# Optimization experiments

Measured on AMD Instinct MI355X. Metric: run time of the kernel, lower is better.

The kernel has to match this reference:

```python
import jax, jax.numpy as jnp
import numpy as np

BN_EPS = 1e-5

def conv1x1(x, w, b):
    # x: [B,C,H,W], w: [O,C], b: [O] -> [B,O,H,W]
    return jnp.einsum('bchw,oc->bohw', x, w) + b[None, :, None, None]

def maxpool2x2(x):
    B, C, H, W = x.shape
    return x.reshape(B, C, H // 2, 2, W // 2, 2).max(axis=(3, 5))

def setup_inputs() -> dict:
    key = jax.random.key(0)
    ks = jax.random.split(key, 12)
    B, C, Ci, H, W = 8, 256, 128, 64, 64
    s_in = 1.0 / np.sqrt(C)
    s_mid = 1.0 / np.sqrt(Ci)
    return {
        'x': jax.random.normal(ks[0], (B, C, H, W), jnp.float32),
        'y': jax.random.normal(ks[1], (B, C, H, W), jnp.float32),
        'theta_w': jax.random.normal(ks[2], (Ci, C), jnp.float32) * s_in,
        'theta_b': jax.random.normal(ks[3], (Ci,), jnp.float32) * s_in,
        'phi_w': jax.random.normal(ks[4], (Ci, C), jnp.float32) * s_in,
        'phi_b': jax.random.normal(ks[5], (Ci,), jnp.float32) * s_in,
        'g_w': jax.random.normal(ks[6], (Ci, C), jnp.float32) * s_in,
        'g_b': jax.random.normal(ks[7], (Ci,), jnp.float32) * s_in,
        'w_w': jax.random.normal(ks[8], (C, Ci), jnp.float32) * s_mid,
        'w_b': jax.random.normal(ks[9], (C,), jnp.float32) * s_mid,
        'bn_gamma': jax.random.normal(ks[10], (C,), jnp.float32),
        'bn_beta': jax.random.normal(ks[11], (C,), jnp.float32),
    }

def reference(x, y, theta_w, theta_b, phi_w, phi_b, g_w, g_b, w_w, w_b, bn_gamma, bn_beta):
    B, C, H, W = x.shape
    Ci = theta_w.shape[0]
    # Q: [B, N, Ci] from x (no subsample)
    theta_x = conv1x1(x, theta_w, theta_b).reshape(B, Ci, H * W).transpose(0, 2, 1)
    # K: [B, Ci, M] and V: [B, M, Ci] from y (2x2 maxpool subsample)
    phi_x = maxpool2x2(conv1x1(y, phi_w, phi_b)).reshape(B, Ci, -1)
    g_x = maxpool2x2(conv1x1(y, g_w, g_b)).reshape(B, Ci, -1).transpose(0, 2, 1)
    # unscaled dot-product attention, softmax over keys
    f = jnp.einsum('bnc,bcm->bnm', theta_x, phi_x)        # [B, N, M]
    attn = jax.nn.softmax(f, axis=-1)
    out = jnp.einsum('bnm,bmc->bnc', attn, g_x)            # [B, N, Ci]
    out = out.transpose(0, 2, 1).reshape(B, Ci, H, W)
    # W projection (1x1 conv) + BatchNorm (batch statistics, training mode)
    wy = conv1x1(out, w_w, w_b)
    mean = wy.mean(axis=(0, 2, 3))
    var = wy.var(axis=(0, 2, 3))
    wy = (wy - mean[None, :, None, None]) * jax.lax.rsqrt(var[None, :, None, None] + BN_EPS)
    wy = wy * bn_gamma[None, :, None, None] + bn_beta[None, :, None, None]
    return wy + x
```

## Files before the change

### kernel.cpp

```cpp
#include <hip/hip_runtime.h>

#define B_  8
#define C_  256
#define CI_ 128
#define N_  4096
#define M_  1024

typedef unsigned short u16;
typedef _Float16 f16;
typedef __attribute__((ext_vector_type(8))) short short8;
typedef __attribute__((ext_vector_type(8))) _Float16 half8;
typedef __attribute__((ext_vector_type(4))) _Float16 half4;
typedef __attribute__((ext_vector_type(4))) float f32x4;

__device__ __forceinline__ u16 f2bf(float f) {
    unsigned int u = __float_as_uint(f);
    u += 0x7fffu + ((u >> 16) & 1u);
    return (u16)(u >> 16);
}
__device__ __forceinline__ float bf2f(u16 h) {
    return __uint_as_float(((unsigned int)h) << 16);
}

__global__ __launch_bounds__(256) void prep_w_kernel(
    const float* __restrict__ tw, const float* __restrict__ pw,
    const float* __restrict__ gw, const float* __restrict__ ww,
    f16* __restrict__ out_h)
{
    int t = blockIdx.x * 256 + threadIdx.x;
    int wsel = t >> 12, idx = t & 4095;
    int lane = idx & 63;
    const float* src; int F, Cdim;
    if (wsel == 3)      { src = ww; F = 16; Cdim = 128; }
    else if (wsel == 0) { src = tw; F = 8;  Cdim = 256; }
    else if (wsel == 1) { src = pw; F = 8;  Cdim = 256; }
    else                { src = gw; F = 8;  Cdim = 256; }
    int fk = idx >> 6;
    int ks = fk / F, f = fk - ks * F;
    int o = f * 16 + (lane & 15);
    int c = ks * 32 + (lane >> 4) * 8;
    const float* s = src + (size_t)o * Cdim + c;
    float4 v0 = *(const float4*)s;
    float4 v1 = *(const float4*)(s + 4);
    half8 hv;
    hv[0] = (f16)v0.x; hv[1] = (f16)v0.y; hv[2] = (f16)v0.z; hv[3] = (f16)v0.w;
    hv[4] = (f16)v1.x; hv[5] = (f16)v1.y; hv[6] = (f16)v1.z; hv[7] = (f16)v1.w;
    size_t oo = (size_t)wsel * 32768 + (size_t)idx * 8;
    *(half8*)&out_h[oo] = hv;
}

__global__ __launch_bounds__(256) void qconv_kernel(
    const float* __restrict__ x,
    const f16* __restrict__ Bfh, const float* __restrict__ bias,
    f16* __restrict__ qh_out)
{
    const int tid = threadIdx.x;
    const int wave = tid >> 6, lane = tid & 63;
    const int tx = lane & 15, quad = lane >> 4;
    const int ot = blockIdx.y, b = blockIdx.z;
    const int nw = blockIdx.x * 64 + wave * 16;

    f32x4 acc[4];
    #pragma unroll
    for (int i = 0; i < 4; ++i) acc[i] = (f32x4){0.f, 0.f, 0.f, 0.f};

    #pragma unroll
    for (int ks = 0; ks < 8; ++ks) {
        const size_t cbase = ((size_t)b * C_ + ks * 32 + quad * 8) * N_ + nw + tx;
        float a[8];
        #pragma unroll
        for (int j = 0; j < 8; ++j) a[j] = x[cbase + (size_t)j * N_];
        half8 ah;
        #pragma unroll
        for (int j = 0; j < 8; ++j) ah[j] = (f16)a[j];
        #pragma unroll
        for (int fi = 0; fi < 4; ++fi) {
            int f = ot * 4 + fi;
            size_t bo = ((size_t)(ks * 8 + f) * 64 + lane) * 8;
            half8 bh = *(const half8*)&Bfh[bo];
            acc[fi] = __builtin_amdgcn_mfma_f32_16x16x32_f16(ah, bh, acc[fi], 0, 0, 0);
        }
    }

    #pragma unroll
    for (int fi = 0; fi < 4; ++fi) {
        int f = ot * 4 + fi;
        float bv = bias[f * 16 + tx];
        #pragma unroll
        for (int r = 0; r < 4; ++r) {
            size_t addr = ((size_t)(b * N_ + nw + quad * 4 + r)) * CI_ + f * 16 + tx;
            qh_out[addr] = (f16)(acc[fi][r] + bv);
        }
    }
}

__global__ __launch_bounds__(256) void kvconv_kernel(
    const float* __restrict__ y,
    const f16* __restrict__ PfH, const f16* __restrict__ GfH,
    const float* __restrict__ phib, const float* __restrict__ gb,
    f16* __restrict__ khi, u16* __restrict__ vf)
{
    const int tid = threadIdx.x;
    const int w = tid >> 6, lane = tid & 63;
    const int tx = lane & 15, quad = lane >> 4;
    const int t = blockIdx.x, ot = blockIdx.y, b = blockIdx.z;

    const size_t nA = (size_t)t * 128 + w * 16 + tx;
    const size_t nB = nA + 64;

    f32x4 accP[2][4], accG[2][4];
    #pragma unroll
    for (int i = 0; i < 2; ++i)
        #pragma unroll
        for (int j = 0; j < 4; ++j) {
            accP[i][j] = (f32x4){0.f, 0.f, 0.f, 0.f};
            accG[i][j] = (f32x4){0.f, 0.f, 0.f, 0.f};
        }

    #pragma unroll
    for (int ks = 0; ks < 8; ++ks) {
        const size_t cbase = ((size_t)b * C_ + ks * 32 + quad * 8) * N_;
        float a0[8], a1[8];
        #pragma unroll
        for (int j = 0; j < 8; ++j) {
            a0[j] = y[cbase + (size_t)j * N_ + nA];
            a1[j] = y[cbase + (size_t)j * N_ + nB];
        }
        half8 ah0, ah1;
        #pragma unroll
        for (int j = 0; j < 8; ++j) {
            ah0[j] = (f16)a0[j];
            ah1[j] = (f16)a1[j];
        }
        #pragma unroll
        for (int of = 0; of < 4; ++of) {
            int f = ot * 4 + of;
            size_t bo = ((size_t)(ks * 8 + f) * 64 + lane) * 8;
            half8 ph = *(const half8*)&PfH[bo];
            half8 gh = *(const half8*)&GfH[bo];
            accP[0][of] = __builtin_amdgcn_mfma_f32_16x16x32_f16(ah0, ph, accP[0][of], 0, 0, 0);
            accP[1][of] = __builtin_amdgcn_mfma_f32_16x16x32_f16(ah1, ph, accP[1][of], 0, 0, 0);
            accG[0][of] = __builtin_amdgcn_mfma_f32_16x16x32_f16(ah0, gh, accG[0][of], 0, 0, 0);
            accG[1][of] = __builtin_amdgcn_mfma_f32_16x16x32_f16(ah1, gh, accG[1][of], 0, 0, 0);
        }
    }

    #pragma unroll
    for (int of = 0; of < 4; ++of) {
        int ci = (ot * 4 + of) * 16 + tx;
        float pb = phib[ci], gbv = gb[ci];
        #pragma unroll
        for (int j = 0; j < 2; ++j) {
            float vP = fmaxf(fmaxf(accP[0][of][2 * j], accP[0][of][2 * j + 1]),
                             fmaxf(accP[1][of][2 * j], accP[1][of][2 * j + 1])) + pb;
            float vG = fmaxf(fmaxf(accG[0][of][2 * j], accG[0][of][2 * j + 1]),
                             fmaxf(accG[1][of][2 * j], accG[1][of][2 * j + 1])) + gbv;
            int mm = 8 * w + 2 * quad + j;
            int fragK = (mm >> 4) * 4 + (ci >> 5);
            int laneK = (((ci & 31) >> 3) << 4) + (mm & 15);
            size_t ka = (((size_t)(b * 32 + t) * 8 + fragK) * 64 + laneK) * 8 + (ci & 7);
            khi[ka] = (f16)vP;
            int fragV = ci >> 4;
            size_t va = (((size_t)(b * 32 + t) * 8 + fragV) * 64 + w * 16 + tx) * 8 + (2 * quad + j);
            vf[va] = f2bf(vG);
        }
    }
}

__global__ __launch_bounds__(256) void attn_kernel(
    const f16* __restrict__ Qh, const f16* __restrict__ Kf,
    const u16* __restrict__ Vf, f16* __restrict__ OP, float* __restrict__ L)
{
    __shared__ __align__(16) f16 kh_sh[4096];
    __shared__ __align__(16) u16 vf_sh[4096];
    __shared__ __align__(16) u16 p_sh[4][16 * 40];

    const int tid = threadIdx.x;
    const int wave = tid >> 6, lane = tid & 63;
    const int tx = lane & 15, quad = lane >> 4;
    const int half = blockIdx.y, b = blockIdx.z;
    const int q0 = blockIdx.x * 64 + wave * 16;
    const float FM = 48.f;

    half8 qh[4];
    {
        const f16* qp = Qh + ((size_t)b * N_ + q0 + tx) * CI_ + quad * 8;
        #pragma unroll
        for (int ks = 0; ks < 4; ++ks) qh[ks] = *(const half8*)&qp[ks * 32];
    }

    f32x4 acc[8];
    #pragma unroll
    for (int f = 0; f < 8; ++f) acc[f] = (f32x4){0.f, 0.f, 0.f, 0.f};
    float lrun[4] = {0.f, 0.f, 0.f, 0.f};

    const f16* Khb = Kf + ((size_t)b * 32 + half * 16) * 4096;
    const u16* Vb  = Vf + ((size_t)b * 32 + half * 16) * 4096;

    half8 rk[2]; short8 rv[2];
    #pragma unroll
    for (int rp = 0; rp < 2; ++rp) {
        int idx = (tid + 256 * rp) * 8;
        rk[rp] = *(const half8*)&Khb[idx];
        rv[rp] = *(const short8*)&Vb[idx];
    }

    for (int ch = 0; ch < 16; ++ch) {
        __syncthreads();
        #pragma unroll
        for (int rp = 0; rp < 2; ++rp) {
            int idx = (tid + 256 * rp) * 8;
            *(half8*)&kh_sh[idx] = rk[rp];
            *(short8*)&vf_sh[idx] = rv[rp];
        }
        if (ch + 1 < 16) {
            #pragma unroll
            for (int rp = 0; rp < 2; ++rp) {
                int idx = (tid + 256 * rp) * 8;
                rk[rp] = *(const half8*)&Khb[(ch + 1) * 4096 + idx];
                rv[rp] = *(const short8*)&Vb[(ch + 1) * 4096 + idx];
            }
        }
        __syncthreads();

        f32x4 s0 = (f32x4){0.f, 0.f, 0.f, 0.f};
        f32x4 s1 = (f32x4){0.f, 0.f, 0.f, 0.f};
        #pragma unroll
        for (int ks = 0; ks < 4; ++ks) {
            half8 bh0 = *(const half8*)&kh_sh[ks * 512 + lane * 8];
            half8 bh1 = *(const half8*)&kh_sh[(4 + ks) * 512 + lane * 8];
            s0 = __builtin_amdgcn_mfma_f32_16x16x32_f16(qh[ks], bh0, s0, 0, 0, 0);
            s1 = __builtin_amdgcn_mfma_f32_16x16x32_f16(qh[ks], bh1, s1, 0, 0, 0);
        }

        u16* pw_ = p_sh[wave];
        #pragma unroll
        for (int r = 0; r < 4; ++r) {
            float p0 = __expf(s0[r] - FM);
            float p1 = __expf(s1[r] - FM);
            lrun[r] += p0 + p1;
            pw_[(4 * quad + r) * 40 + tx]      = f2bf(p0);
            pw_[(4 * quad + r) * 40 + 16 + tx] = f2bf(p1);
        }
        asm volatile("s_waitcnt lgkmcnt(0)" ::: "memory");
        short8 pf = *(const short8*)&pw_[tx * 40 + quad * 8];

        #pragma unroll
        for (int f = 0; f < 8; ++f) {
            short8 vb = *(const short8*)&vf_sh[f * 512 + lane * 8];
            acc[f] = __builtin_amdgcn_mfma_f32_16x16x32_bf16(pf, vb, acc[f], 0, 0, 0);
        }
    }

    #pragma unroll
    for (int d = 1; d < 16; d <<= 1) {
        #pragma unroll
        for (int r = 0; r < 4; ++r) lrun[r] += __shfl_xor(lrun[r], d);
    }
    if (tx == 0) {
        #pragma unroll
        for (int r = 0; r < 4; ++r)
            L[(size_t)half * 32768 + b * N_ + q0 + 4 * quad + r] = lrun[r];
    }
    float inv[4];
    #pragma unroll
    for (int r = 0; r < 4; ++r) inv[r] = 1.f / lrun[r];
    f16* Ob = OP + ((size_t)half * B_ + b) * N_ * CI_ + (size_t)q0 * CI_;
    #pragma unroll
    for (int f = 0; f < 8; ++f) {
        #pragma unroll
        for (int r = 0; r < 4; ++r)
            Ob[(size_t)(4 * quad + r) * CI_ + f * 16 + tx] = (f16)(acc[f][r] * inv[r]);
    }
}

__global__ __launch_bounds__(256) void attn_merge_kernel(
    const f16* __restrict__ OP, const float* __restrict__ L,
    f16* __restrict__ Oh)
{
    int gid = blockIdx.x * 256 + threadIdx.x;
    size_t base = (size_t)gid * 4;
    int row = (int)(base >> 7);
    float l0 = L[row], l1 = L[32768 + row];
    float invs = 1.f / (l0 + l1);
    float w0 = l0 * invs, w1 = l1 * invs;
    half4 a = *(const half4*)&OP[base];
    half4 c = *(const half4*)&OP[4194304 + base];
    half4 o;
    o[0] = (f16)((float)a[0] * w0 + (float)c[0] * w1);
    o[1] = (f16)((float)a[1] * w0 + (float)c[1] * w1);
    o[2] = (f16)((float)a[2] * w0 + (float)c[2] * w1);
    o[3] = (f16)((float)a[3] * w0 + (float)c[3] * w1);
    *(half4*)&Oh[base] = o;
}

__global__ __launch_bounds__(256) void wconv_mfma_kernel(
    const f16* __restrict__ Bh, const f16* __restrict__ Afh,
    const float* __restrict__ bias, f16* __restrict__ wy,
    float* __restrict__ part)
{
    const int tid = threadIdx.x;
    const int wave = tid >> 6, lane = tid & 63;
    const int tx = lane & 15, quad = lane >> 4;
    const int id = blockIdx.x;
    const int xcd = id & 7;
    const int s = id >> 3;
    const int ot = s & 1;
    const int gnt = (s >> 1) * 8 + xcd;
    const int b = gnt >> 7;
    const int n0 = (gnt & 127) * 32;
    const int of0 = ot * 8 + wave * 2, of1 = of0 + 1;

    half8 wah[4][2];
    #pragma unroll
    for (int ks = 0; ks < 4; ++ks) {
        #pragma unroll
        for (int ff = 0; ff < 2; ++ff) {
            size_t aa = ((size_t)(ks * 16 + of0 + ff) * 64 + lane) * 8;
            wah[ks][ff] = *(const half8*)&Afh[aa];
        }
    }

    f32x4 acc[2][2];
    #pragma unroll
    for (int i = 0; i < 2; ++i)
        #pragma unroll
        for (int j = 0; j < 2; ++j) acc[i][j] = (f32x4){0.f, 0.f, 0.f, 0.f};

    #pragma unroll
    for (int ks = 0; ks < 4; ++ks) {
        half8 bh[2];
        #pragma unroll
        for (int nf = 0; nf < 2; ++nf) {
            size_t ba = ((size_t)(b * N_ + n0 + nf * 16 + tx)) * CI_ + ks * 32 + quad * 8;
            bh[nf] = *(const half8*)&Bh[ba];
        }
        #pragma unroll
        for (int ff = 0; ff < 2; ++ff)
            #pragma unroll
            for (int nf = 0; nf < 2; ++nf)
                acc[ff][nf] = __builtin_amdgcn_mfma_f32_16x16x32_f16(wah[ks][ff], bh[nf], acc[ff][nf], 0, 0, 0);
    }

    #pragma unroll
    for (int ff = 0; ff < 2; ++ff) {
        int fg = ff ? of1 : of0;
        #pragma unroll
        for (int r = 0; r < 4; ++r) {
            int o = fg * 16 + quad * 4 + r;
            float bo = bias[o];
            float ps = 0.f, pss = 0.f;
            #pragma unroll
            for (int nf = 0; nf < 2; ++nf) {
                float v = acc[ff][nf][r] + bo;
                wy[((size_t)b * C_ + o) * N_ + n0 + nf * 16 + tx] = (f16)v;
                ps += v; pss += v * v;
            }
            #pragma unroll
            for (int d = 1; d < 16; d <<= 1) {
                ps  += __shfl_xor(ps, d);
                pss += __shfl_xor(pss, d);
            }
            if (tx == 0) {
                part[(size_t)o * 1024 + gnt]          = ps;
                part[262144 + (size_t)o * 1024 + gnt] = pss;
            }
        }
    }
}

__global__ __launch_bounds__(256) void bn_reduce_kernel(
    const float* __restrict__ part, float* __restrict__ sums)
{
    int w = blockIdx.x * 4 + (threadIdx.x >> 6);
    int lane = threadIdx.x & 63;
    int p = w >> 8, o = w & 255;
    const float* src = part + (size_t)p * 262144 + (size_t)o * 1024;
    float s = 0.f;
    #pragma unroll
    for (int j = 0; j < 16; ++j) s += src[j * 64 + lane];
    #pragma unroll
    for (int d = 1; d < 64; d <<= 1) s += __shfl_xor(s, d);
    if (lane == 0) sums[p * 256 + o] = s;
}

__global__ __launch_bounds__(256) void bn_final_kernel(
    const f16* __restrict__ wy, const float* __restrict__ x,
    const float* __restrict__ gsum, const float* __restrict__ gsumsq,
    const float* __restrict__ gamma, const float* __restrict__ beta,
    float* __restrict__ out)
{
    int idx = blockIdx.x * 256 + threadIdx.x;
    size_t base = (size_t)idx * 4;
    int o = (int)((base >> 12) & 255);
    half4 wv = *(const half4*)&wy[base];
    float4 xv = *(const float4*)&x[base];
    const float invc = 1.f / 32768.f;
    float mean = gsum[o] * invc;
    float var  = gsumsq[o] * invc - mean * mean;
    float sc = gamma[o] * rsqrtf(var + 1e-5f);
    float sh = beta[o] - mean * sc;
    float4 r;
    r.x = (float)wv[0] * sc + sh + xv.x;
    r.y = (float)wv[1] * sc + sh + xv.y;
    r.z = (float)wv[2] * sc + sh + xv.z;
    r.w = (float)wv[3] * sc + sh + xv.w;
    *(float4*)&out[base] = r;
}

extern "C" void kernel_launch(void* const* d_in, const int* in_sizes, int n_in,
                              void* d_out, int out_size, void* d_ws, size_t ws_size,
                              hipStream_t stream) {
    (void)in_sizes; (void)n_in; (void)out_size; (void)ws_size;
    const float* x       = (const float*)d_in[0];
    const float* y       = (const float*)d_in[1];
    const float* theta_w = (const float*)d_in[2];
    const float* theta_b = (const float*)d_in[3];
    const float* phi_w   = (const float*)d_in[4];
    const float* phi_b   = (const float*)d_in[5];
    const float* g_w     = (const float*)d_in[6];
    const float* g_b     = (const float*)d_in[7];
    const float* w_w     = (const float*)d_in[8];
    const float* w_b     = (const float*)d_in[9];
    const float* bn_g    = (const float*)d_in[10];
    const float* bn_b    = (const float*)d_in[11];
    float* out = (float*)d_out;

    float* ws = (float*)d_ws;
    f16*   Qh   = (f16*)(ws);
    f16*   Kf   = (f16*)(ws + 2097152);
    u16*   Vfp  = (u16*)(ws + 2621440);
    f16*   OP   = (f16*)(ws + 3145728);
    float* L    = ws + 7340032;
    f16*   Oh   = (f16*)(ws + 7405568);
    f16*   WY   = (f16*)(ws + 9502720);
    float* PART = ws + 13697024;
    f16*   Wfh  = (f16*)(ws + 14221312);
    float* SUMS = ws + 14286848;

    prep_w_kernel<<<64, 256, 0, stream>>>(theta_w, phi_w, g_w, w_w, Wfh);

    qconv_kernel<<<dim3(64, 2, 8), 256, 0, stream>>>(x, Wfh, theta_b, Qh);
    kvconv_kernel<<<dim3(32, 2, 8), 256, 0, stream>>>(
        y, Wfh + 32768, Wfh + 65536, phi_b, g_b, Kf, Vfp);

    attn_kernel<<<dim3(64, 2, 8), 256, 0, stream>>>(Qh, Kf, Vfp, OP, L);
    attn_merge_kernel<<<4096, 256, 0, stream>>>(OP, L, Oh);

    wconv_mfma_kernel<<<2048, 256, 0, stream>>>(Oh, Wfh + 98304, w_b, WY, PART);
    bn_reduce_kernel<<<128, 256, 0, stream>>>(PART, SUMS);
    bn_final_kernel<<<8192, 256, 0, stream>>>(WY, x, SUMS, SUMS + 256, bn_g, bn_b, out);
}
```

Before: 215.0 us.

## Drop split-K attention and merge kernel; remap conv block indices for XCD locality

The attention kernel now walks all 32 key/value chunks in one block instead of splitting them into two halves. That removes the partial-output buffers, the row-sum buffer and the separate merge kernel. The wconv kernel now computes all 256 output channels per block, with 4 fragments per wave, so each Oh tile is loaded once instead of twice. The q/kv conv kernels switch to a 1D grid with an index remap that groups blocks sharing a batch and n-tile onto the same XCD. The trade-off is half as many attention blocks, each doing twice the serial work, which lowers occupancy and parallelism on the many-CU device.

```diff
diff --git a/kernel.cpp b/kernel.cpp
--- a/kernel.cpp
+++ b/kernel.cpp
@@ -57,8 +57,12 @@
     const int tid = threadIdx.x;
     const int wave = tid >> 6, lane = tid & 63;
     const int tx = lane & 15, quad = lane >> 4;
-    const int ot = blockIdx.y, b = blockIdx.z;
-    const int nw = blockIdx.x * 64 + wave * 16;
+    const int id = blockIdx.x;
+    const int ot = (id >> 3) & 1;
+    const int p  = (id & 7) | ((id >> 4) << 3);
+    const int nb = p & 63;
+    const int b  = p >> 6;
+    const int nw = nb * 64 + wave * 16;
 
     f32x4 acc[4];
     #pragma unroll
@@ -103,7 +107,11 @@
     const int tid = threadIdx.x;
     const int w = tid >> 6, lane = tid & 63;
     const int tx = lane & 15, quad = lane >> 4;
-    const int t = blockIdx.x, ot = blockIdx.y, b = blockIdx.z;
+    const int id = blockIdx.x;
+    const int ot = (id >> 3) & 1;
+    const int p  = (id & 7) | ((id >> 4) << 3);
+    const int t = p & 31;
+    const int b = p >> 5;
 
     const size_t nA = (size_t)t * 128 + w * 16 + tx;
     const size_t nB = nA + 64;
@@ -169,7 +177,7 @@
 
 __global__ __launch_bounds__(256) void attn_kernel(
     const f16* __restrict__ Qh, const f16* __restrict__ Kf,
-    const u16* __restrict__ Vf, f16* __restrict__ OP, float* __restrict__ L)
+    const u16* __restrict__ Vf, f16* __restrict__ Oh)
 {
     __shared__ __align__(16) f16 kh_sh[4096];
     __shared__ __align__(16) u16 vf_sh[4096];
@@ -178,7 +186,7 @@
     const int tid = threadIdx.x;
     const int wave = tid >> 6, lane = tid & 63;
     const int tx = lane & 15, quad = lane >> 4;
-    const int half = blockIdx.y, b = blockIdx.z;
+    const int b = blockIdx.y;
     const int q0 = blockIdx.x * 64 + wave * 16;
     const float FM = 48.f;
 
@@ -194,8 +202,8 @@
     for (int f = 0; f < 8; ++f) acc[f] = (f32x4){0.f, 0.f, 0.f, 0.f};
     float lrun[4] = {0.f, 0.f, 0.f, 0.f};
 
-    const f16* Khb = Kf + ((size_t)b * 32 + half * 16) * 4096;
-    const u16* Vb  = Vf + ((size_t)b * 32 + half * 16) * 4096;
+    const f16* Khb = Kf + (size_t)b * 32 * 4096;
+    const u16* Vb  = Vf + (size_t)b * 32 * 4096;
 
     half8 rk[2]; short8 rv[2];
     #pragma unroll
@@ -205,7 +213,7 @@
         rv[rp] = *(const short8*)&Vb[idx];
     }
 
-    for (int ch = 0; ch < 16; ++ch) {
+    for (int ch = 0; ch < 32; ++ch) {
         __syncthreads();
         #pragma unroll
         for (int rp = 0; rp < 2; ++rp) {
@@ -213,7 +221,7 @@
             *(half8*)&kh_sh[idx] = rk[rp];
             *(short8*)&vf_sh[idx] = rv[rp];
         }
-        if (ch + 1 < 16) {
+        if (ch + 1 < 32) {
             #pragma unroll
             for (int rp = 0; rp < 2; ++rp) {
                 int idx = (tid + 256 * rp) * 8;
@@ -257,41 +265,16 @@
         #pragma unroll
         for (int r = 0; r < 4; ++r) lrun[r] += __shfl_xor(lrun[r], d);
     }
-    if (tx == 0) {
-        #pragma unroll
-        for (int r = 0; r < 4; ++r)
-            L[(size_t)half * 32768 + b * N_ + q0 + 4 * quad + r] = lrun[r];
-    }
     float inv[4];
     #pragma unroll
     for (int r = 0; r < 4; ++r) inv[r] = 1.f / lrun[r];
-    f16* Ob = OP + ((size_t)half * B_ + b) * N_ * CI_ + (size_t)q0 * CI_;
+    f16* Ob = Oh + ((size_t)b * N_ + q0) * CI_;
     #pragma unroll
     for (int f = 0; f < 8; ++f) {
         #pragma unroll
         for (int r = 0; r < 4; ++r)
             Ob[(size_t)(4 * quad + r) * CI_ + f * 16 + tx] = (f16)(acc[f][r] * inv[r]);
     }
-}
-
-__global__ __launch_bounds__(256) void attn_merge_kernel(
-    const f16* __restrict__ OP, const float* __restrict__ L,
-    f16* __restrict__ Oh)
-{
-    int gid = blockIdx.x * 256 + threadIdx.x;
-    size_t base = (size_t)gid * 4;
-    int row = (int)(base >> 7);
-    float l0 = L[row], l1 = L[32768 + row];
-    float invs = 1.f / (l0 + l1);
-    float w0 = l0 * invs, w1 = l1 * invs;
-    half4 a = *(const half4*)&OP[base];
-    half4 c = *(const half4*)&OP[4194304 + base];
-    half4 o;
-    o[0] = (f16)((float)a[0] * w0 + (float)c[0] * w1);
-    o[1] = (f16)((float)a[1] * w0 + (float)c[1] * w1);
-    o[2] = (f16)((float)a[2] * w0 + (float)c[2] * w1);
-    o[3] = (f16)((float)a[3] * w0 + (float)c[3] * w1);
-    *(half4*)&Oh[base] = o;
 }
 
 __global__ __launch_bounds__(256) void wconv_mfma_kernel(
@@ -302,28 +285,24 @@
     const int tid = threadIdx.x;
     const int wave = tid >> 6, lane = tid & 63;
     const int tx = lane & 15, quad = lane >> 4;
-    const int id = blockIdx.x;
-    const int xcd = id & 7;
-    const int s = id >> 3;
-    const int ot = s & 1;
-    const int gnt = (s >> 1) * 8 + xcd;
+    const int gnt = blockIdx.x;
     const int b = gnt >> 7;
     const int n0 = (gnt & 127) * 32;
-    const int of0 = ot * 8 + wave * 2, of1 = of0 + 1;
-
-    half8 wah[4][2];
+    const int of0 = wave * 4;
+
+    half8 wah[4][4];
     #pragma unroll
     for (int ks = 0; ks < 4; ++ks) {
         #pragma unroll
-        for (int ff = 0; ff < 2; ++ff) {
+        for (int ff = 0; ff < 4; ++ff) {
             size_t aa = ((size_t)(ks * 16 + of0 + ff) * 64 + lane) * 8;
             wah[ks][ff] = *(const half8*)&Afh[aa];
         }
     }
 
-    f32x4 acc[2][2];
-    #pragma unroll
-    for (int i = 0; i < 2; ++i)
+    f32x4 acc[4][2];
+    #pragma unroll
+    for (int i = 0; i < 4; ++i)
         #pragma unroll
         for (int j = 0; j < 2; ++j) acc[i][j] = (f32x4){0.f, 0.f, 0.f, 0.f};
 
@@ -336,15 +315,15 @@
             bh[nf] = *(const half8*)&Bh[ba];
         }
         #pragma unroll
-        for (int ff = 0; ff < 2; ++ff)
+        for (int ff = 0; ff < 4; ++ff)
             #pragma unroll
             for (int nf = 0; nf < 2; ++nf)
                 acc[ff][nf] = __builtin_amdgcn_mfma_f32_16x16x32_f16(wah[ks][ff], bh[nf], acc[ff][nf], 0, 0, 0);
     }
 
     #pragma unroll
-    for (int ff = 0; ff < 2; ++ff) {
-        int fg = ff ? of1 : of0;
+    for (int ff = 0; ff < 4; ++ff) {
+        int fg = of0 + ff;
         #pragma unroll
         for (int r = 0; r < 4; ++r) {
             int o = fg * 16 + quad * 4 + r;
@@ -430,8 +409,6 @@
     f16*   Qh   = (f16*)(ws);
     f16*   Kf   = (f16*)(ws + 2097152);
     u16*   Vfp  = (u16*)(ws + 2621440);
-    f16*   OP   = (f16*)(ws + 3145728);
-    float* L    = ws + 7340032;
     f16*   Oh   = (f16*)(ws + 7405568);
     f16*   WY   = (f16*)(ws + 9502720);
     float* PART = ws + 13697024;
@@ -440,14 +417,13 @@
 
     prep_w_kernel<<<64, 256, 0, stream>>>(theta_w, phi_w, g_w, w_w, Wfh);
 
-    qconv_kernel<<<dim3(64, 2, 8), 256, 0, stream>>>(x, Wfh, theta_b, Qh);
-    kvconv_kernel<<<dim3(32, 2, 8), 256, 0, stream>>>(
+    qconv_kernel<<<1024, 256, 0, stream>>>(x, Wfh, theta_b, Qh);
+    kvconv_kernel<<<512, 256, 0, stream>>>(
         y, Wfh + 32768, Wfh + 65536, phi_b, g_b, Kf, Vfp);
 
-    attn_kernel<<<dim3(64, 2, 8), 256, 0, stream>>>(Qh, Kf, Vfp, OP, L);
-    attn_merge_kernel<<<4096, 256, 0, stream>>>(OP, L, Oh);
-
-    wconv_mfma_kernel<<<2048, 256, 0, stream>>>(Oh, Wfh + 98304, w_b, WY, PART);
+    attn_kernel<<<dim3(64, 8), 256, 0, stream>>>(Qh, Kf, Vfp, Oh);
+
+    wconv_mfma_kernel<<<1024, 256, 0, stream>>>(Oh, Wfh + 98304, w_b, WY, PART);
     bn_reduce_kernel<<<128, 256, 0, stream>>>(PART, SUMS);
     bn_final_kernel<<<8192, 256, 0, stream>>>(WY, x, SUMS, SUMS + 256, bn_g, bn_b, out);
 }
```

Result: faster. 208.0 us (-3.3%).
